# Kernel optimization log

Measured on AMD Instinct MI355X. Metric: run time of the kernel, lower is better.

## Reference

```python
import jax, jax.numpy as jnp
import numpy as np

NFEAT = 256
N_HEAD = 8
CTXS = (31, 61)
HPS = N_HEAD // len(CTXS)  # heads per scale = 4


def _scale_out(query, value, W1, W2, W3, ctx):
    # query, value: [B, T, F]; W1: [F, F]; W2: [F, HPS*ctx]; W3: [F, F]
    B, T, F = query.shape
    q = jnp.maximum(query @ W1, 0.0)                      # relu(w1(query))
    attn = jax.nn.softmax((q @ W2).reshape(B, T, HPS, ctx), axis=-1)  # [B,T,HPS,ctx]
    half = (ctx - 1) // 2
    v = jnp.pad(value @ W3, ((0, 0), (half, half), (0, 0)))  # [B, T+ctx-1, F]
    idx = jnp.arange(T)[:, None] + jnp.arange(ctx)[None, :]  # [T, ctx] window indices
    vw = v[:, idx]                                          # [B, T, ctx, F]
    vw = vw.reshape(B, T, ctx, HPS, F // HPS)               # per-head dim = F/HPS
    out = jnp.einsum('bthc,btchd->bthd', attn, vw)          # [B,T,HPS,F/HPS]
    return out.reshape(B, T, F)


def setup_inputs() -> dict:
    key = jax.random.key(0)
    ks = jax.random.split(key, 12)
    B, T, F = 2, 4096, NFEAT
    s = 0.02
    return {
        'query': jax.random.normal(ks[0], (B, T, F), jnp.float32),
        'key':   jax.random.normal(ks[1], (B, T, F), jnp.float32),
        'value': jax.random.normal(ks[2], (B, T, F), jnp.float32),
        'w1_0': jax.random.normal(ks[3], (F, F), jnp.float32) * s,
        'w1_1': jax.random.normal(ks[4], (F, F), jnp.float32) * s,
        'w2_0': jax.random.normal(ks[5], (F, HPS * CTXS[0]), jnp.float32) * s,
        'w2_1': jax.random.normal(ks[6], (F, HPS * CTXS[1]), jnp.float32) * s,
        'w3_0': jax.random.normal(ks[7], (F, F), jnp.float32) * s,
        'w3_1': jax.random.normal(ks[8], (F, F), jnp.float32) * s,
        'scale_w': jnp.ones((2,), jnp.float32) / 2.0,
        'w_out': jax.random.normal(ks[9], (F, F), jnp.float32) * s,
    }


def reference(query, key, value, w1_0, w1_1, w2_0, w2_1, w3_0, w3_1, scale_w, w_out):
    sw = jax.nn.softmax(scale_w)
    out = sw[0] * _scale_out(query, value, w1_0, w2_0, w3_0, CTXS[0])
    out = out + sw[1] * _scale_out(query, value, w1_1, w2_1, w3_1, CTXS[1])
    return out @ w_out
```

## Files before the change

### kernel.cpp

```cpp
#include <hip/hip_runtime.h>
#include <hip/hip_bf16.h>
#include <type_traits>

static constexpr int BATCH = 2;
static constexpr int T     = 4096;
static constexpr int F     = 256;
static constexpr int M     = BATCH * T;
static constexpr int K     = 256;
static constexpr int HPS   = 4;
static constexpr int CTX0  = 31, CTX1 = 61;
static constexpr int N2_0  = HPS * CTX0;
static constexpr int N2_1  = HPS * CTX1;

typedef short bf16x8 __attribute__((ext_vector_type(8)));
typedef float f32x4  __attribute__((ext_vector_type(4)));

__device__ __forceinline__ ushort f2bf(float f) {
    union { float f; uint u; } v; v.f = f;
    uint u = v.u;
    return (ushort)((u + 0x7fffu + ((u >> 16) & 1u)) >> 16);
}
__device__ __forceinline__ float asf(uint u) {
    union { uint u; float f; } v; v.u = u; return v.f;
}

__global__ __launch_bounds__(256) void cvtqv_kernel(
    const float* __restrict__ q, const float* __restrict__ v,
    ushort* __restrict__ qb, ushort* __restrict__ vb)
{
    const float* src = blockIdx.y ? v : q;
    ushort*      dst = blockIdx.y ? vb : qb;
    size_t i = ((size_t)blockIdx.x * 256 + threadIdx.x) * 8;
    float4 a = *reinterpret_cast<const float4*>(src + i);
    float4 b = *reinterpret_cast<const float4*>(src + i + 4);
    ushort o[8] = { f2bf(a.x), f2bf(a.y), f2bf(a.z), f2bf(a.w),
                    f2bf(b.x), f2bf(b.y), f2bf(b.z), f2bf(b.w) };
    *reinterpret_cast<bf16x8*>(dst + i) = *reinterpret_cast<bf16x8*>(o);
}

struct WcvtArgs {
    const float* w1_0; const float* w1_1;
    const float* w2_0; const float* w2_1;
    const float* w3_0; const float* w3_1;
    const float* wo;
    ushort* wt;
};
static constexpr int WT_ROWS = 512 + N2_0 + N2_1 + 512 + 256;

__global__ __launch_bounds__(256) void wcvt_kernel(WcvtArgs a) {
    int gid = blockIdx.x * 256 + threadIdx.x;
    if (gid >= WT_ROWS * (K / 8)) return;
    int row = gid >> 5;
    int kk  = (gid & 31) * 8;

    const float* src; int stride, col;
    if (row < 512) {
        int n = row;
        if (n < 256) { src = a.w1_0; col = n; } else { src = a.w1_1; col = n - 256; }
        stride = 256;
    } else if (row < 512 + N2_0) {
        src = a.w2_0; col = row - 512; stride = N2_0;
    } else if (row < 512 + N2_0 + N2_1) {
        src = a.w2_1; col = row - (512 + N2_0); stride = N2_1;
    } else if (row < 512 + N2_0 + N2_1 + 512) {
        int n = row - (512 + N2_0 + N2_1);
        if (n < 256) { src = a.w3_0; col = n; } else { src = a.w3_1; col = n - 256; }
        stride = 256;
    } else {
        src = a.wo; col = row - (512 + N2_0 + N2_1 + 512); stride = 256;
    }

    ushort o[8];
#pragma unroll
    for (int j = 0; j < 8; j++) o[j] = f2bf(src[(size_t)(kk + j) * stride + col]);
    *reinterpret_cast<bf16x8*>(a.wt + (size_t)row * K + kk) =
        *reinterpret_cast<bf16x8*>(o);
}

template <typename OutT, bool RELU>
__global__ __launch_bounds__(256) void gemm_kernel(
    const ushort* __restrict__ A,
    int lda,
    const ushort* __restrict__ Bt,
    OutT*         __restrict__ C,
    int N, int ncb)
{
    __shared__ ushort Al[64][256];
    __shared__ ushort Bl[64][256];

    const int tid = threadIdx.x;
    const int nwg = gridDim.x;
    const int lin = blockIdx.x;
    const int qq  = nwg >> 3;
    const int swz = (lin & 7) * qq + (lin >> 3);
    const int cb  = swz % ncb;
    const int rb  = swz / ncb;
    const int m0  = rb * 64;
    const int n0  = cb * 64;

    for (int idx = tid; idx < 64 * 32; idx += 256) {
        int row = idx >> 5, ch = idx & 31;
        bf16x8 v = *reinterpret_cast<const bf16x8*>(A + (size_t)(m0 + row) * lda + ch * 8);
        *reinterpret_cast<bf16x8*>(&Al[row][(ch ^ (row & 7)) * 8]) = v;
    }
    for (int idx = tid; idx < 64 * 32; idx += 256) {
        int row = idx >> 5, ch = idx & 31;
        bf16x8 v = {};
        if (n0 + row < N)
            v = *reinterpret_cast<const bf16x8*>(Bt + (size_t)(n0 + row) * K + ch * 8);
        *reinterpret_cast<bf16x8*>(&Bl[row][(ch ^ (row & 7)) * 8]) = v;
    }

    const int wave = tid >> 6, lane = tid & 63;
    const int wr = wave >> 1, wc = wave & 1;
    const int l15 = lane & 15, l4 = lane >> 4;

    f32x4 acc[2][2] = {};
    __syncthreads();

#pragma unroll
    for (int s = 0; s < 8; s++) {
        bf16x8 af[2], bfr[2];
#pragma unroll
        for (int i = 0; i < 2; i++) {
            int row = wr * 32 + i * 16 + l15;
            int ch  = (s * 4 + l4) ^ (row & 7);
            af[i] = *reinterpret_cast<const bf16x8*>(&Al[row][ch * 8]);
        }
#pragma unroll
        for (int j = 0; j < 2; j++) {
            int row = wc * 32 + j * 16 + l15;
            int ch  = (s * 4 + l4) ^ (row & 7);
            bfr[j] = *reinterpret_cast<const bf16x8*>(&Bl[row][ch * 8]);
        }
#pragma unroll
        for (int i = 0; i < 2; i++)
#pragma unroll
            for (int j = 0; j < 2; j++)
                acc[i][j] = __builtin_amdgcn_mfma_f32_16x16x32_bf16(af[i], bfr[j], acc[i][j], 0, 0, 0);
    }

#pragma unroll
    for (int i = 0; i < 2; i++)
#pragma unroll
        for (int j = 0; j < 2; j++) {
            int col = n0 + wc * 32 + j * 16 + l15;
            if (col < N) {
#pragma unroll
                for (int r = 0; r < 4; r++) {
                    int row = m0 + wr * 32 + i * 16 + l4 * 4 + r;
                    float v = acc[i][j][r];
                    if (RELU) v = fmaxf(v, 0.0f);
                    if constexpr (std::is_same<OutT, ushort>::value)
                        C[(size_t)row * N + col] = f2bf(v);
                    else
                        C[(size_t)row * N + col] = v;
                }
            }
        }
}

__global__ __launch_bounds__(256) void attn_kernel(
    const float*  __restrict__ lg0,
    const float*  __restrict__ lg1,
    const ushort* __restrict__ v01,
    const float*  __restrict__ scale_w,
    ushort*       __restrict__ outc)
{
    const int tid = threadIdx.x;
    const int nwg = gridDim.x;
    const int lin = blockIdx.x;
    const int qq  = nwg >> 3;
    const int swz = (lin & 7) * qq + (lin >> 3);
    const int bt0 = swz * 8;
    const int b   = bt0 >> 12;
    const int t0  = bt0 & (T - 1);

    __shared__ float  attw[8][368];
    __shared__ ushort v0l[38][256];
    __shared__ ushort v1l[68][256];

    for (int idx = tid; idx < 1216 + 2176; idx += 256) {
        ushort* dst; int tt, srccol;
        if (idx < 1216) {
            int row = idx >> 5, ch = idx & 31;
            dst = &v0l[row][ch * 8]; tt = t0 - 15 + row; srccol = ch * 8;
        } else {
            int i2 = idx - 1216;
            int row = i2 >> 5, ch = i2 & 31;
            dst = &v1l[row][ch * 8]; tt = t0 - 30 + row; srccol = 256 + ch * 8;
        }
        bf16x8 v = {};
        if ((unsigned)tt < (unsigned)T)
            v = *reinterpret_cast<const bf16x8*>(v01 + ((size_t)(b * T + tt) * 512 + srccol));
        *reinterpret_cast<bf16x8*>(dst) = v;
    }

    float s0 = scale_w[0], s1 = scale_w[1];
    float mxs = fmaxf(s0, s1);
    float e0 = __expf(s0 - mxs), e1 = __expf(s1 - mxs);
    float sw0 = e0 / (e0 + e1), sw1 = e1 / (e0 + e1);

    {
        int task = tid >> 2, sub = tid & 3;
        int tok = task >> 3, rest = task & 7;
        int scale = rest >> 2, h = rest & 3;
        int bt = bt0 + tok;
        const float* lp; float* dst; int ctx; float sw;
        if (scale == 0) {
            lp = lg0 + (size_t)bt * N2_0 + h * CTX0;
            dst = &attw[tok][h * CTX0]; ctx = CTX0; sw = sw0;
        } else {
            lp = lg1 + (size_t)bt * N2_1 + h * CTX1;
            dst = &attw[tok][124 + h * CTX1]; ctx = CTX1; sw = sw1;
        }
        float mx = -1e30f;
        for (int c = sub; c < ctx; c += 4) mx = fmaxf(mx, lp[c]);
        mx = fmaxf(mx, __shfl_xor(mx, 1));
        mx = fmaxf(mx, __shfl_xor(mx, 2));
        float s = 0.f;
        for (int c = sub; c < ctx; c += 4) {
            float e = __expf(lp[c] - mx);
            dst[c] = e; s += e;
        }
        s += __shfl_xor(s, 1);
        s += __shfl_xor(s, 2);
        float scl = sw / s;
        for (int c = sub; c < ctx; c += 4) dst[c] *= scl;
    }
    __syncthreads();

    const int tok = tid >> 5;
    const int f0  = (tid & 31) * 8;
    const int h   = f0 >> 6;

    float acc[8] = {};
    const float* a0 = &attw[tok][h * CTX0];
    const float* a1 = &attw[tok][124 + h * CTX1];

#pragma unroll 4
    for (int c = 0; c < CTX0; c++) {
        float w = a0[c];
        uint4 u = *reinterpret_cast<const uint4*>(&v0l[tok + c][f0]);
        acc[0] += w * asf(u.x << 16); acc[1] += w * asf(u.x & 0xffff0000u);
        acc[2] += w * asf(u.y << 16); acc[3] += w * asf(u.y & 0xffff0000u);
        acc[4] += w * asf(u.z << 16); acc[5] += w * asf(u.z & 0xffff0000u);
        acc[6] += w * asf(u.w << 16); acc[7] += w * asf(u.w & 0xffff0000u);
    }
#pragma unroll 4
    for (int c = 0; c < CTX1; c++) {
        float w = a1[c];
        uint4 u = *reinterpret_cast<const uint4*>(&v1l[tok + c][f0]);
        acc[0] += w * asf(u.x << 16); acc[1] += w * asf(u.x & 0xffff0000u);
        acc[2] += w * asf(u.y << 16); acc[3] += w * asf(u.y & 0xffff0000u);
        acc[4] += w * asf(u.z << 16); acc[5] += w * asf(u.z & 0xffff0000u);
        acc[6] += w * asf(u.w << 16); acc[7] += w * asf(u.w & 0xffff0000u);
    }

    ushort o[8];
#pragma unroll
    for (int j = 0; j < 8; j++) o[j] = f2bf(acc[j]);
    *reinterpret_cast<bf16x8*>(outc + (size_t)(bt0 + tok) * F + f0) =
        *reinterpret_cast<bf16x8*>(o);
}

extern "C" void kernel_launch(void* const* d_in, const int* in_sizes, int n_in,
                              void* d_out, int out_size, void* d_ws, size_t ws_size,
                              hipStream_t stream)
{
    const float* Q    = (const float*)d_in[0];
    const float* V    = (const float*)d_in[2];
    const float* W1_0 = (const float*)d_in[3];
    const float* W1_1 = (const float*)d_in[4];
    const float* W2_0 = (const float*)d_in[5];
    const float* W2_1 = (const float*)d_in[6];
    const float* W3_0 = (const float*)d_in[7];
    const float* W3_1 = (const float*)d_in[8];
    const float* SW   = (const float*)d_in[9];
    const float* WO   = (const float*)d_in[10];

    char* p = (char*)d_ws;
    auto carve = [&](size_t bytes) { char* r = p; p += (bytes + 255) & ~255ull; return r; };
    ushort* wt   = (ushort*)carve((size_t)WT_ROWS * K * 2);
    ushort* qbf  = (ushort*)carve((size_t)M * K * 2);
    ushort* vbf  = (ushort*)carve((size_t)M * K * 2);
    ushort* q01  = (ushort*)carve((size_t)M * 512 * 2);
    float*  lg0  = (float*) carve((size_t)M * N2_0 * 4);
    float*  lg1  = (float*) carve((size_t)M * N2_1 * 4);
    ushort* v01  = (ushort*)carve((size_t)M * 512 * 2);
    ushort* ocb  = (ushort*)carve((size_t)M * F * 2);
    (void)ws_size;

    const ushort* w1t  = wt;
    const ushort* w2t0 = wt + (size_t)512 * K;
    const ushort* w2t1 = wt + (size_t)(512 + N2_0) * K;
    const ushort* w3t  = wt + (size_t)(512 + N2_0 + N2_1) * K;
    const ushort* wot  = wt + (size_t)(512 + N2_0 + N2_1 + 512) * K;

    {
        dim3 g(M * K / 8 / 256, 2);
        cvtqv_kernel<<<g, 256, 0, stream>>>(Q, V, qbf, vbf);
        int nthread = WT_ROWS * (K / 8);
        wcvt_kernel<<<(nthread + 255) / 256, 256, 0, stream>>>(
            WcvtArgs{ W1_0, W1_1, W2_0, W2_1, W3_0, W3_1, WO, wt });
    }

    gemm_kernel<ushort, true ><<<(M/64) * 8, 256, 0, stream>>>(qbf, K, w1t, q01, 512, 8);
    gemm_kernel<float,  false><<<(M/64) * 2, 256, 0, stream>>>(q01,       512, w2t0, lg0, N2_0, 2);
    gemm_kernel<float,  false><<<(M/64) * 4, 256, 0, stream>>>(q01 + 256, 512, w2t1, lg1, N2_1, 4);
    gemm_kernel<ushort, false><<<(M/64) * 8, 256, 0, stream>>>(vbf, K, w3t, v01, 512, 8);
    attn_kernel<<<M / 8, 256, 0, stream>>>(lg0, lg1, v01, SW, ocb);
    gemm_kernel<float,  false><<<(M/64) * 4, 256, 0, stream>>>(ocb, K, wot, (float*)d_out, F, 4);
}
```

Baseline: 170.8 us.

## Fuse input bf16 conversion into GEMMs, merge W2 GEMMs, split attention per scale

Removes the standalone Q/V fp32-to-bf16 conversion kernel and converts the A operand on load inside the GEMM. The two W2 logit GEMMs become one K=512 GEMM against a block-diagonal weight padded to 384 columns. The GEMM now stages K in 128-wide chunks to halve LDS use and raise occupancy. Attention is split into two per-scale kernels that each handle 32 tokens, which reduces halo reloads; the two partial outputs are summed while loading the output-projection GEMM. The cost is wasted MACs on the zero blocks of the merged W2 GEMM and an extra bf16 rounding of each partial sum before it is added.

```diff
diff --git a/kernel.cpp b/kernel.cpp
--- a/kernel.cpp
+++ b/kernel.cpp
@@ -6,11 +6,9 @@
 static constexpr int T     = 4096;
 static constexpr int F     = 256;
 static constexpr int M     = BATCH * T;
-static constexpr int K     = 256;
 static constexpr int HPS   = 4;
 static constexpr int CTX0  = 31, CTX1 = 61;
-static constexpr int N2_0  = HPS * CTX0;
-static constexpr int N2_1  = HPS * CTX1;
+static constexpr int LGN   = 384;
 
 typedef short bf16x8 __attribute__((ext_vector_type(8)));
 typedef float f32x4  __attribute__((ext_vector_type(4)));
@@ -23,20 +21,13 @@
 __device__ __forceinline__ float asf(uint u) {
     union { uint u; float f; } v; v.u = u; return v.f;
 }
-
-__global__ __launch_bounds__(256) void cvtqv_kernel(
-    const float* __restrict__ q, const float* __restrict__ v,
-    ushort* __restrict__ qb, ushort* __restrict__ vb)
-{
-    const float* src = blockIdx.y ? v : q;
-    ushort*      dst = blockIdx.y ? vb : qb;
-    size_t i = ((size_t)blockIdx.x * 256 + threadIdx.x) * 8;
-    float4 a = *reinterpret_cast<const float4*>(src + i);
-    float4 b = *reinterpret_cast<const float4*>(src + i + 4);
-    ushort o[8] = { f2bf(a.x), f2bf(a.y), f2bf(a.z), f2bf(a.w),
-                    f2bf(b.x), f2bf(b.y), f2bf(b.z), f2bf(b.w) };
-    *reinterpret_cast<bf16x8*>(dst + i) = *reinterpret_cast<bf16x8*>(o);
-}
+__device__ __forceinline__ float bf2f(ushort u) { return asf(((uint)u) << 16); }
+
+static constexpr size_t W1T_OFF  = 0;
+static constexpr size_t W2B_OFF  = W1T_OFF + (size_t)512 * 256;
+static constexpr size_t W3T_OFF  = W2B_OFF + (size_t)384 * 512;
+static constexpr size_t WOT_OFF  = W3T_OFF + (size_t)512 * 256;
+static constexpr size_t WT_ELEMS = WOT_OFF + (size_t)256 * 256;
 
 struct WcvtArgs {
     const float* w1_0; const float* w1_1;
@@ -45,48 +36,55 @@
     const float* wo;
     ushort* wt;
 };
-static constexpr int WT_ROWS = 512 + N2_0 + N2_1 + 512 + 256;
 
 __global__ __launch_bounds__(256) void wcvt_kernel(WcvtArgs a) {
     int gid = blockIdx.x * 256 + threadIdx.x;
-    if (gid >= WT_ROWS * (K / 8)) return;
-    int row = gid >> 5;
-    int kk  = (gid & 31) * 8;
-
-    const float* src; int stride, col;
-    if (row < 512) {
-        int n = row;
-        if (n < 256) { src = a.w1_0; col = n; } else { src = a.w1_1; col = n - 256; }
-        stride = 256;
-    } else if (row < 512 + N2_0) {
-        src = a.w2_0; col = row - 512; stride = N2_0;
-    } else if (row < 512 + N2_0 + N2_1) {
-        src = a.w2_1; col = row - (512 + N2_0); stride = N2_1;
-    } else if (row < 512 + N2_0 + N2_1 + 512) {
-        int n = row - (512 + N2_0 + N2_1);
-        if (n < 256) { src = a.w3_0; col = n; } else { src = a.w3_1; col = n - 256; }
-        stride = 256;
+    if (gid >= (int)(WT_ELEMS / 8)) return;
+    ushort o[8];
+    if (gid < 16384 || (gid >= 16384 + 24576 && gid < 16384 + 24576 + 16384)) {
+        bool w3 = gid >= 16384;
+        int g = w3 ? gid - (16384 + 24576) : gid;
+        int row = g >> 5;
+        int kk  = (g & 31) * 8;
+        const float* src = (row < 256) ? (w3 ? a.w3_0 : a.w1_0) : (w3 ? a.w3_1 : a.w1_1);
+        int col = row & 255;
+#pragma unroll
+        for (int j = 0; j < 8; j++) o[j] = f2bf(src[(size_t)(kk + j) * 256 + col]);
+        size_t base = (w3 ? W3T_OFF : W1T_OFF) + (size_t)row * 256 + kk;
+        *reinterpret_cast<bf16x8*>(a.wt + base) = *reinterpret_cast<bf16x8*>(o);
+    } else if (gid < 16384 + 24576) {
+        int g = gid - 16384;
+        int row = g >> 6;
+        int kk  = (g & 63) * 8;
+#pragma unroll
+        for (int j = 0; j < 8; j++) {
+            int k = kk + j;
+            float v = 0.f;
+            if (row < 124) { if (k < 256) v = a.w2_0[(size_t)k * 124 + row]; }
+            else if (row < 368) { if (k >= 256) v = a.w2_1[(size_t)(k - 256) * 244 + (row - 124)]; }
+            o[j] = f2bf(v);
+        }
+        *reinterpret_cast<bf16x8*>(a.wt + W2B_OFF + (size_t)row * 512 + kk) =
+            *reinterpret_cast<bf16x8*>(o);
     } else {
-        src = a.wo; col = row - (512 + N2_0 + N2_1 + 512); stride = 256;
-    }
-
-    ushort o[8];
-#pragma unroll
-    for (int j = 0; j < 8; j++) o[j] = f2bf(src[(size_t)(kk + j) * stride + col]);
-    *reinterpret_cast<bf16x8*>(a.wt + (size_t)row * K + kk) =
-        *reinterpret_cast<bf16x8*>(o);
-}
-
-template <typename OutT, bool RELU>
-__global__ __launch_bounds__(256) void gemm_kernel(
-    const ushort* __restrict__ A,
-    int lda,
+        int g = gid - (16384 + 24576 + 16384);
+        int row = g >> 5;
+        int kk  = (g & 31) * 8;
+#pragma unroll
+        for (int j = 0; j < 8; j++) o[j] = f2bf(a.wo[(size_t)(kk + j) * 256 + row]);
+        *reinterpret_cast<bf16x8*>(a.wt + WOT_OFF + (size_t)row * 256 + kk) =
+            *reinterpret_cast<bf16x8*>(o);
+    }
+}
+
+template <int KTOT, int AMODE, typename OutT, bool RELU>
+__global__ __launch_bounds__(256, 4) void gemm_kernel(
+    const void* __restrict__ Av, const void* __restrict__ A2v, int lda,
     const ushort* __restrict__ Bt,
-    OutT*         __restrict__ C,
-    int N, int ncb)
+    OutT* __restrict__ C, int N, int ncb)
 {
-    __shared__ ushort Al[64][256];
-    __shared__ ushort Bl[64][256];
+    __shared__ ushort Al[64][128];
+    __shared__ ushort Bl[64][128];
 
     const int tid = threadIdx.x;
     const int nwg = gridDim.x;
@@ -98,46 +96,75 @@
     const int m0  = rb * 64;
     const int n0  = cb * 64;
 
-    for (int idx = tid; idx < 64 * 32; idx += 256) {
-        int row = idx >> 5, ch = idx & 31;
-        bf16x8 v = *reinterpret_cast<const bf16x8*>(A + (size_t)(m0 + row) * lda + ch * 8);
-        *reinterpret_cast<bf16x8*>(&Al[row][(ch ^ (row & 7)) * 8]) = v;
-    }
-    for (int idx = tid; idx < 64 * 32; idx += 256) {
-        int row = idx >> 5, ch = idx & 31;
-        bf16x8 v = {};
-        if (n0 + row < N)
-            v = *reinterpret_cast<const bf16x8*>(Bt + (size_t)(n0 + row) * K + ch * 8);
-        *reinterpret_cast<bf16x8*>(&Bl[row][(ch ^ (row & 7)) * 8]) = v;
-    }
+    const ushort* Ab  = (const ushort*)Av;
+    const float*  Af  = (const float*)Av;
+    const ushort* A2b = (const ushort*)A2v;
 
     const int wave = tid >> 6, lane = tid & 63;
     const int wr = wave >> 1, wc = wave & 1;
     const int l15 = lane & 15, l4 = lane >> 4;
 
     f32x4 acc[2][2] = {};
-    __syncthreads();
-
-#pragma unroll
-    for (int s = 0; s < 8; s++) {
-        bf16x8 af[2], bfr[2];
-#pragma unroll
-        for (int i = 0; i < 2; i++) {
-            int row = wr * 32 + i * 16 + l15;
-            int ch  = (s * 4 + l4) ^ (row & 7);
-            af[i] = *reinterpret_cast<const bf16x8*>(&Al[row][ch * 8]);
-        }
-#pragma unroll
-        for (int j = 0; j < 2; j++) {
-            int row = wc * 32 + j * 16 + l15;
-            int ch  = (s * 4 + l4) ^ (row & 7);
-            bfr[j] = *reinterpret_cast<const bf16x8*>(&Bl[row][ch * 8]);
-        }
-#pragma unroll
-        for (int i = 0; i < 2; i++)
-#pragma unroll
-            for (int j = 0; j < 2; j++)
-                acc[i][j] = __builtin_amdgcn_mfma_f32_16x16x32_bf16(af[i], bfr[j], acc[i][j], 0, 0, 0);
+
+    for (int kh = 0; kh < KTOT / 128; kh++) {
+#pragma unroll
+        for (int it = 0; it < 4; it++) {
+            int i = it * 256 + tid;
+            int row = i >> 4, ch = i & 15;
+            int k = kh * 128 + ch * 8;
+            bf16x8 v;
+            if constexpr (AMODE == 0) {
+                v = *reinterpret_cast<const bf16x8*>(Ab + (size_t)(m0 + row) * lda + k);
+            } else if constexpr (AMODE == 1) {
+                const float* ap = Af + (size_t)(m0 + row) * lda + k;
+                float4 x = *reinterpret_cast<const float4*>(ap);
+                float4 y = *reinterpret_cast<const float4*>(ap + 4);
+                ushort o[8] = { f2bf(x.x), f2bf(x.y), f2bf(x.z), f2bf(x.w),
+                                f2bf(y.x), f2bf(y.y), f2bf(y.z), f2bf(y.w) };
+                v = *reinterpret_cast<bf16x8*>(o);
+            } else {
+                bf16x8 p = *reinterpret_cast<const bf16x8*>(Ab  + (size_t)(m0 + row) * lda + k);
+                bf16x8 q = *reinterpret_cast<const bf16x8*>(A2b + (size_t)(m0 + row) * lda + k);
+                ushort o[8];
+#pragma unroll
+                for (int j = 0; j < 8; j++)
+                    o[j] = f2bf(bf2f((ushort)p[j]) + bf2f((ushort)q[j]));
+                v = *reinterpret_cast<bf16x8*>(o);
+            }
+            *reinterpret_cast<bf16x8*>(&Al[row][(ch ^ (row & 7)) * 8]) = v;
+        }
+#pragma unroll
+        for (int it = 0; it < 4; it++) {
+            int i = it * 256 + tid;
+            int row = i >> 4, ch = i & 15;
+            int k = kh * 128 + ch * 8;
+            bf16x8 v = *reinterpret_cast<const bf16x8*>(Bt + (size_t)(n0 + row) * KTOT + k);
+            *reinterpret_cast<bf16x8*>(&Bl[row][(ch ^ (row & 7)) * 8]) = v;
+        }
+        __syncthreads();
+
+#pragma unroll
+        for (int s = 0; s < 4; s++) {
+            bf16x8 af[2], bfr[2];
+#pragma unroll
+            for (int i = 0; i < 2; i++) {
+                int row = wr * 32 + i * 16 + l15;
+                int ch  = (s * 4 + l4) ^ (row & 7);
+                af[i] = *reinterpret_cast<const bf16x8*>(&Al[row][ch * 8]);
+            }
+#pragma unroll
+            for (int j = 0; j < 2; j++) {
+                int row = wc * 32 + j * 16 + l15;
+                int ch  = (s * 4 + l4) ^ (row & 7);
+                bfr[j] = *reinterpret_cast<const bf16x8*>(&Bl[row][ch * 8]);
+            }
+#pragma unroll
+            for (int i = 0; i < 2; i++)
+#pragma unroll
+                for (int j = 0; j < 2; j++)
+                    acc[i][j] = __builtin_amdgcn_mfma_f32_16x16x32_bf16(af[i], bfr[j], acc[i][j], 0, 0, 0);
+        }
+        __syncthreads();
     }
 
 #pragma unroll
@@ -145,123 +172,102 @@
 #pragma unroll
         for (int j = 0; j < 2; j++) {
             int col = n0 + wc * 32 + j * 16 + l15;
-            if (col < N) {
-#pragma unroll
-                for (int r = 0; r < 4; r++) {
-                    int row = m0 + wr * 32 + i * 16 + l4 * 4 + r;
-                    float v = acc[i][j][r];
-                    if (RELU) v = fmaxf(v, 0.0f);
-                    if constexpr (std::is_same<OutT, ushort>::value)
-                        C[(size_t)row * N + col] = f2bf(v);
-                    else
-                        C[(size_t)row * N + col] = v;
-                }
+#pragma unroll
+            for (int r = 0; r < 4; r++) {
+                int row = m0 + wr * 32 + i * 16 + l4 * 4 + r;
+                float v = acc[i][j][r];
+                if (RELU) v = fmaxf(v, 0.0f);
+                if constexpr (std::is_same<OutT, ushort>::value)
+                    C[(size_t)row * N + col] = f2bf(v);
+                else
+                    C[(size_t)row * N + col] = v;
             }
         }
 }
 
+template <int SCALE>
 __global__ __launch_bounds__(256) void attn_kernel(
-    const float*  __restrict__ lg0,
-    const float*  __restrict__ lg1,
+    const float*  __restrict__ lg,
     const ushort* __restrict__ v01,
     const float*  __restrict__ scale_w,
-    ushort*       __restrict__ outc)
+    ushort*       __restrict__ p)
 {
+    constexpr int CTX  = SCALE ? CTX1 : CTX0;
+    constexpr int HALO = (CTX - 1) / 2;
+    constexpr int VR   = 32 + 2 * HALO;
+    constexpr int LGO  = SCALE ? 124 : 0;
+    constexpr int VOFF = SCALE ? 256 : 0;
+
+    __shared__ ushort vl[VR][256];
+    __shared__ float  att[32][HPS * CTX];
+
     const int tid = threadIdx.x;
     const int nwg = gridDim.x;
     const int lin = blockIdx.x;
     const int qq  = nwg >> 3;
     const int swz = (lin & 7) * qq + (lin >> 3);
-    const int bt0 = swz * 8;
+    const int bt0 = swz * 32;
     const int b   = bt0 >> 12;
     const int t0  = bt0 & (T - 1);
 
-    __shared__ float  attw[8][368];
-    __shared__ ushort v0l[38][256];
-    __shared__ ushort v1l[68][256];
-
-    for (int idx = tid; idx < 1216 + 2176; idx += 256) {
-        ushort* dst; int tt, srccol;
-        if (idx < 1216) {
-            int row = idx >> 5, ch = idx & 31;
-            dst = &v0l[row][ch * 8]; tt = t0 - 15 + row; srccol = ch * 8;
-        } else {
-            int i2 = idx - 1216;
-            int row = i2 >> 5, ch = i2 & 31;
-            dst = &v1l[row][ch * 8]; tt = t0 - 30 + row; srccol = 256 + ch * 8;
-        }
+    for (int i = tid; i < VR * 32; i += 256) {
+        int row = i >> 5, ch = i & 31;
+        int tt = t0 - HALO + row;
         bf16x8 v = {};
         if ((unsigned)tt < (unsigned)T)
-            v = *reinterpret_cast<const bf16x8*>(v01 + ((size_t)(b * T + tt) * 512 + srccol));
-        *reinterpret_cast<bf16x8*>(dst) = v;
+            v = *reinterpret_cast<const bf16x8*>(
+                v01 + ((size_t)(b * T + tt) * 512 + VOFF + ch * 8));
+        *reinterpret_cast<bf16x8*>(&vl[row][ch * 8]) = v;
     }
 
     float s0 = scale_w[0], s1 = scale_w[1];
     float mxs = fmaxf(s0, s1);
     float e0 = __expf(s0 - mxs), e1 = __expf(s1 - mxs);
-    float sw0 = e0 / (e0 + e1), sw1 = e1 / (e0 + e1);
+    float sw = (SCALE ? e1 : e0) / (e0 + e1);
 
     {
-        int task = tid >> 2, sub = tid & 3;
-        int tok = task >> 3, rest = task & 7;
-        int scale = rest >> 2, h = rest & 3;
-        int bt = bt0 + tok;
-        const float* lp; float* dst; int ctx; float sw;
-        if (scale == 0) {
-            lp = lg0 + (size_t)bt * N2_0 + h * CTX0;
-            dst = &attw[tok][h * CTX0]; ctx = CTX0; sw = sw0;
-        } else {
-            lp = lg1 + (size_t)bt * N2_1 + h * CTX1;
-            dst = &attw[tok][124 + h * CTX1]; ctx = CTX1; sw = sw1;
-        }
+        int task = tid >> 1, sub = tid & 1;
+        int tok = task >> 2, h = task & 3;
+        const float* lp = lg + (size_t)(bt0 + tok) * LGN + LGO + h * CTX;
+        float* dst = &att[tok][h * CTX];
         float mx = -1e30f;
-        for (int c = sub; c < ctx; c += 4) mx = fmaxf(mx, lp[c]);
+        for (int c = sub; c < CTX; c += 2) mx = fmaxf(mx, lp[c]);
         mx = fmaxf(mx, __shfl_xor(mx, 1));
-        mx = fmaxf(mx, __shfl_xor(mx, 2));
         float s = 0.f;
-        for (int c = sub; c < ctx; c += 4) {
+        for (int c = sub; c < CTX; c += 2) {
             float e = __expf(lp[c] - mx);
             dst[c] = e; s += e;
         }
         s += __shfl_xor(s, 1);
-        s += __shfl_xor(s, 2);
         float scl = sw / s;
-        for (int c = sub; c < ctx; c += 4) dst[c] *= scl;
+        for (int c = sub; c < CTX; c += 2) dst[c] *= scl;
     }
     __syncthreads();
 
-    const int tok = tid >> 5;
-    const int f0  = (tid & 31) * 8;
-    const int h   = f0 >> 6;
-
-    float acc[8] = {};
-    const float* a0 = &attw[tok][h * CTX0];
-    const float* a1 = &attw[tok][124 + h * CTX1];
-
+    const int w  = tid >> 5;
+    const int f0 = (tid & 31) * 8;
+    const int h  = f0 >> 6;
+
+#pragma unroll 1
+    for (int tk = 0; tk < 4; tk++) {
+        int tok = tk * 8 + w;
+        const float* aw = &att[tok][h * CTX];
+        float acc[8] = {};
 #pragma unroll 4
-    for (int c = 0; c < CTX0; c++) {
-        float w = a0[c];
-        uint4 u = *reinterpret_cast<const uint4*>(&v0l[tok + c][f0]);
-        acc[0] += w * asf(u.x << 16); acc[1] += w * asf(u.x & 0xffff0000u);
-        acc[2] += w * asf(u.y << 16); acc[3] += w * asf(u.y & 0xffff0000u);
-        acc[4] += w * asf(u.z << 16); acc[5] += w * asf(u.z & 0xffff0000u);
-        acc[6] += w * asf(u.w << 16); acc[7] += w * asf(u.w & 0xffff0000u);
-    }
-#pragma unroll 4
-    for (int c = 0; c < CTX1; c++) {
-        float w = a1[c];
-        uint4 u = *reinterpret_cast<const uint4*>(&v1l[tok + c][f0]);
-        acc[0] += w * asf(u.x << 16); acc[1] += w * asf(u.x & 0xffff0000u);
-        acc[2] += w * asf(u.y << 16); acc[3] += w * asf(u.y & 0xffff0000u);
-        acc[4] += w * asf(u.z << 16); acc[5] += w * asf(u.z & 0xffff0000u);
-        acc[6] += w * asf(u.w << 16); acc[7] += w * asf(u.w & 0xffff0000u);
-    }
-
-    ushort o[8];
-#pragma unroll
-    for (int j = 0; j < 8; j++) o[j] = f2bf(acc[j]);
-    *reinterpret_cast<bf16x8*>(outc + (size_t)(bt0 + tok) * F + f0) =
-        *reinterpret_cast<bf16x8*>(o);
+        for (int c = 0; c < CTX; c++) {
+            float wv = aw[c];
+            uint4 u = *reinterpret_cast<const uint4*>(&vl[tok + c][f0]);
+            acc[0] += wv * asf(u.x << 16); acc[1] += wv * asf(u.x & 0xffff0000u);
+            acc[2] += wv * asf(u.y << 16); acc[3] += wv * asf(u.y & 0xffff0000u);
+            acc[4] += wv * asf(u.z << 16); acc[5] += wv * asf(u.z & 0xffff0000u);
+            acc[6] += wv * asf(u.w << 16); acc[7] += wv * asf(u.w & 0xffff0000u);
+        }
+        ushort o[8];
+#pragma unroll
+        for (int j = 0; j < 8; j++) o[j] = f2bf(acc[j]);
+        *reinterpret_cast<bf16x8*>(p + (size_t)(bt0 + tok) * F + f0) =
+            *reinterpret_cast<bf16x8*>(o);
+    }
 }
 
 extern "C" void kernel_launch(void* const* d_in, const int* in_sizes, int n_in,
@@ -279,36 +285,32 @@
     const float* SW   = (const float*)d_in[9];
     const float* WO   = (const float*)d_in[10];
 
-    char* p = (char*)d_ws;
-    auto carve = [&](size_t bytes) { char* r = p; p += (bytes + 255) & ~255ull; return r; };
-    ushort* wt   = (ushort*)carve((size_t)WT_ROWS * K * 2);
-    ushort* qbf  = (ushort*)carve((size_t)M * K * 2);
-    ushort* vbf  = (ushort*)carve((size_t)M * K * 2);
-    ushort* q01  = (ushort*)carve((size_t)M * 512 * 2);
-    float*  lg0  = (float*) carve((size_t)M * N2_0 * 4);
-    float*  lg1  = (float*) carve((size_t)M * N2_1 * 4);
-    ushort* v01  = (ushort*)carve((size_t)M * 512 * 2);
-    ushort* ocb  = (ushort*)carve((size_t)M * F * 2);
+    char* pws = (char*)d_ws;
+    auto carve = [&](size_t bytes) { char* r = pws; pws += (bytes + 255) & ~255ull; return r; };
+    ushort* wt  = (ushort*)carve(WT_ELEMS * 2);
+    ushort* q01 = (ushort*)carve((size_t)M * 512 * 2);
+    float*  lg  = (float*) carve((size_t)M * LGN * 4);
+    ushort* v01 = (ushort*)carve((size_t)M * 512 * 2);
+    ushort* p0  = (ushort*)carve((size_t)M * F * 2);
+    ushort* p1  = (ushort*)carve((size_t)M * F * 2);
     (void)ws_size;
 
-    const ushort* w1t  = wt;
-    const ushort* w2t0 = wt + (size_t)512 * K;
-    const ushort* w2t1 = wt + (size_t)(512 + N2_0) * K;
-    const ushort* w3t  = wt + (size_t)(512 + N2_0 + N2_1) * K;
-    const ushort* wot  = wt + (size_t)(512 + N2_0 + N2_1 + 512) * K;
-
-    {
-        dim3 g(M * K / 8 / 256, 2);
-        cvtqv_kernel<<<g, 256, 0, stream>>>(Q, V, qbf, vbf);
-        int nthread = WT_ROWS * (K / 8);
-        wcvt_kernel<<<(nthread + 255) / 256, 256, 0, stream>>>(
-            WcvtArgs{ W1_0, W1_1, W2_0, W2_1, W3_0, W3_1, WO, wt });
-    }
-
-    gemm_kernel<ushort, true ><<<(M/64) * 8, 256, 0, stream>>>(qbf, K, w1t, q01, 512, 8);
-    gemm_kernel<float,  false><<<(M/64) * 2, 256, 0, stream>>>(q01,       512, w2t0, lg0, N2_0, 2);
-    gemm_kernel<float,  false><<<(M/64) * 4, 256, 0, stream>>>(q01 + 256, 512, w2t1, lg1, N2_1, 4);
-    gemm_kernel<ushort, false><<<(M/64) * 8, 256, 0, stream>>>(vbf, K, w3t, v01, 512, 8);
-    attn_kernel<<<M / 8, 256, 0, stream>>>(lg0, lg1, v01, SW, ocb);
-    gemm_kernel<float,  false><<<(M/64) * 4, 256, 0, stream>>>(ocb, K, wot, (float*)d_out, F, 4);
-}
+    const ushort* w1t   = wt + W1T_OFF;
+    const ushort* w2blk = wt + W2B_OFF;
+    const ushort* w3t   = wt + W3T_OFF;
+    const ushort* wot   = wt + WOT_OFF;
+
+    wcvt_kernel<<<(int)(WT_ELEMS / 8 / 256), 256, 0, stream>>>(
+        WcvtArgs{ W1_0, W1_1, W2_0, W2_1, W3_0, W3_1, WO, wt });
+
+    gemm_kernel<256, 1, ushort, true ><<<(M/64) * 8, 256, 0, stream>>>(
+        Q, nullptr, 256, w1t, q01, 512, 8);
+    gemm_kernel<256, 1, ushort, false><<<(M/64) * 8, 256, 0, stream>>>(
+        V, nullptr, 256, w3t, v01, 512, 8);
+    gemm_kernel<512, 0, float,  false><<<(M/64) * 6, 256, 0, stream>>>(
+        q01, nullptr, 512, w2blk, lg, LGN, 6);
+    attn_kernel<0><<<M / 32, 256, 0, stream>>>(lg, v01, SW, p0);
+    attn_kernel<1><<<M / 32, 256, 0, stream>>>(lg, v01, SW, p1);
+    gemm_kernel<256, 2, float,  false><<<(M/64) * 4, 256, 0, stream>>>(
+        p0, p1, 256, wot, (float*)d_out, 256, 4);
+}
```

Result: faster. 159.1 us (-6.8%).
